# Kernel tuning notes

Hardware: AMD Instinct MI355X
Metric: run time of the kernel (lower is better)

Reference implementation:

```python
import jax, jax.numpy as jnp
import numpy as np

B, P, N, D = 32, 100, 1000, 128
SQRT_D = 11.313708498984761
CLIP = 10.0


def setup_inputs() -> dict:
    key = jax.random.key(0)
    ks = jax.random.split(key, 8)
    s = 1.0 / np.sqrt(D)  # keep k ~ N(0,1) so exp(k) is stable
    return {
        "encoded_nodes": jax.random.normal(ks[0], (B, N, D), jnp.float32),
        "encoded_q1": jax.random.normal(ks[1], (B, P, D), jnp.float32),
        "encoded_last_node": jax.random.normal(ks[2], (B, P, D), jnp.float32),
        "cur_dist": jax.random.uniform(ks[3], (B, P, N), jnp.float32),
        "ninf_mask": jnp.zeros((B, P, N), jnp.float32),
        "log_scale": jnp.ones((1,), jnp.float32),
        "Wq_first": jax.random.normal(ks[4], (D, D), jnp.float32) * s,
        "Wq_last": jax.random.normal(ks[5], (D, D), jnp.float32) * s,
        "Wk": jax.random.normal(ks[6], (D, D), jnp.float32) * s,
        "Wv": jax.random.normal(ks[7], (D, D), jnp.float32) * s,
        "dist_alpha_1": jnp.ones((1,), jnp.float32),
        "AFT_dist_alpha_1": jnp.ones((1,), jnp.float32),
    }


def reference(encoded_nodes, encoded_q1, encoded_last_node, cur_dist, ninf_mask,
              log_scale, Wq_first, Wq_last, Wk, Wv, dist_alpha_1, AFT_dist_alpha_1):
    # set_kv / set_q1 (torch Linear: x @ W.T)
    k = jnp.einsum('bnd,ed->bne', encoded_nodes, Wk)          # [B,N,D]
    v = jnp.einsum('bnd,ed->bne', encoded_nodes, Wv)          # [B,N,D]
    q_first = jnp.einsum('bpd,ed->bpe', encoded_q1, Wq_first) # [B,P,D]
    q_last = jnp.einsum('bpd,ed->bpe', encoded_last_node, Wq_last)
    q = q_first + q_last

    cur_dist_out = -cur_dist                                   # [B,P,N]
    bias_scale = log_scale * AFT_dist_alpha_1 * cur_dist_out + ninf_mask
    ebias = jnp.exp(bias_scale)                                # [B,P,N]
    ek = jnp.exp(k)                                            # [B,N,D]
    num = jnp.einsum('bpn,bnd->bpd', ebias, ek * v)
    den = jnp.einsum('bpn,bnd->bpd', ebias, ek)
    aft_out = jax.nn.sigmoid(q) * (num / den)                  # [B,P,D]

    score = jnp.einsum('bpd,bnd->bpn', aft_out, encoded_nodes) / SQRT_D
    score = score + log_scale * dist_alpha_1 * cur_dist_out
    score = CLIP * jnp.tanh(score) + ninf_mask
    return jax.nn.softmax(score, axis=2)
```

## Files before the change

kernel.cpp:

```cpp
#include <hip/hip_runtime.h>
#include <hip/hip_bf16.h>
#include <math.h>

#define B 32
#define P 100
#define N 1000
#define D 128

constexpr float SQRT_D_INV = 1.0f / 11.313708498984761f;
constexpr float CLIPV = 10.0f;

__device__ __forceinline__ void fma4(float4& a, float s, const float4& b) {
    a.x = fmaf(s, b.x, a.x);
    a.y = fmaf(s, b.y, a.y);
    a.z = fmaf(s, b.z, a.z);
    a.w = fmaf(s, b.w, a.w);
}

#define TT 64
__global__ __launch_bounds__(256) void prep_kernel(
        const float* __restrict__ nodes,
        const float* __restrict__ Wk,  const float* __restrict__ Wv,
        const float* __restrict__ Wqf, const float* __restrict__ Wql,
        float* __restrict__ wkT,  float* __restrict__ wvT,
        float* __restrict__ wqfT, float* __restrict__ wqlT,
        float* __restrict__ nodesT) {
    const int t = threadIdx.x;
    if (blockIdx.x < D) {
        const int e = blockIdx.x;
        const int d = t & 127;
        if ((t >> 7) == 0) {
            wkT[e * D + d] = Wk[d * D + e];
            wvT[e * D + d] = Wv[d * D + e];
        } else {
            wqfT[e * D + d] = Wqf[d * D + e];
            wqlT[e * D + d] = Wql[d * D + e];
        }
        return;
    }
    __shared__ float sh[TT][D + 1];
    const int blk = blockIdx.x - D;
    const int ntiles = (N + TT - 1) / TT;
    const int b  = blk / ntiles;
    const int n0 = (blk % ntiles) * TT;
    const int rows = min(TT, N - n0);

    const float4* src = (const float4*)(nodes + ((long)b * N + n0) * D);
    for (int i = t; i < rows * (D / 4); i += 256) {
        int r = i >> 5, c = i & 31;
        float4 v = src[(long)r * (D / 4) + c];
        sh[r][c * 4 + 0] = v.x; sh[r][c * 4 + 1] = v.y;
        sh[r][c * 4 + 2] = v.z; sh[r][c * 4 + 3] = v.w;
    }
    __syncthreads();

    const int nl = t & 63;
    const int eg = t >> 6;
    if (nl < rows) {
        #pragma unroll
        for (int k = 0; k < 32; ++k) {
            int e = eg * 32 + k;
            nodesT[((long)b * D + e) * N + n0 + nl] = sh[nl][e];
        }
    }
}

#define R1 32
__global__ __launch_bounds__(256) void kv_kernel(
        const float* __restrict__ nodes,
        const float* __restrict__ wkT,
        const float* __restrict__ wvT,
        float* __restrict__ ek,
        float* __restrict__ ekv) {
    __shared__ float sh[R1][D];
    const int t = threadIdx.x;
    const int dq = t & 31;
    const int rl = t >> 5;
    const long row0 = (long)blockIdx.x * R1;

    const float4* src = (const float4*)(nodes + row0 * D);
    float4* dst = (float4*)(&sh[0][0]);
    #pragma unroll
    for (int i = 0; i < (R1 * D / 4) / 256; ++i)
        dst[t + i * 256] = src[t + i * 256];
    __syncthreads();

    float4 ka[4], va[4];
    #pragma unroll
    for (int rr = 0; rr < 4; ++rr) {
        ka[rr] = make_float4(0.f, 0.f, 0.f, 0.f);
        va[rr] = make_float4(0.f, 0.f, 0.f, 0.f);
    }

    const float* wkp = wkT + dq * 4;
    const float* wvp = wvT + dq * 4;

    float4 cwk[4], cwv[4];
    #pragma unroll
    for (int ee = 0; ee < 4; ++ee) {
        cwk[ee] = *(const float4*)(wkp + ee * D);
        cwv[ee] = *(const float4*)(wvp + ee * D);
    }

    for (int e0 = 0; e0 < D; e0 += 4) {
        float4 nwk[4], nwv[4];
        if (e0 + 4 < D) {
            #pragma unroll
            for (int ee = 0; ee < 4; ++ee) {
                nwk[ee] = *(const float4*)(wkp + (e0 + 4 + ee) * D);
                nwv[ee] = *(const float4*)(wvp + (e0 + 4 + ee) * D);
            }
        }
        #pragma unroll
        for (int rr = 0; rr < 4; ++rr) {
            float4 s4 = *(const float4*)(&sh[rl * 4 + rr][e0]);
            fma4(ka[rr], s4.x, cwk[0]); fma4(ka[rr], s4.y, cwk[1]);
            fma4(ka[rr], s4.z, cwk[2]); fma4(ka[rr], s4.w, cwk[3]);
            fma4(va[rr], s4.x, cwv[0]); fma4(va[rr], s4.y, cwv[1]);
            fma4(va[rr], s4.z, cwv[2]); fma4(va[rr], s4.w, cwv[3]);
        }
        #pragma unroll
        for (int ee = 0; ee < 4; ++ee) { cwk[ee] = nwk[ee]; cwv[ee] = nwv[ee]; }
    }

    #pragma unroll
    for (int rr = 0; rr < 4; ++rr) {
        long row = row0 + rl * 4 + rr;
        float4 e4;
        e4.x = __expf(ka[rr].x); e4.y = __expf(ka[rr].y);
        e4.z = __expf(ka[rr].z); e4.w = __expf(ka[rr].w);
        float4 ev;
        ev.x = e4.x * va[rr].x; ev.y = e4.y * va[rr].y;
        ev.z = e4.z * va[rr].z; ev.w = e4.w * va[rr].w;
        *(float4*)(ek + row * D + dq * 4) = e4;
        *(float4*)(ekv + row * D + dq * 4) = ev;
    }
}

#define R2 16
__global__ __launch_bounds__(256) void q_kernel(
        const float* __restrict__ q1,
        const float* __restrict__ qlast,
        const float* __restrict__ wqfT,
        const float* __restrict__ wqlT,
        float* __restrict__ qsig) {
    __shared__ float sh1[R2][D];
    __shared__ float sh2[R2][D];
    const int t = threadIdx.x;
    const int dq = t & 31;
    const int rl = t >> 5;
    const long row0 = (long)blockIdx.x * R2;

    const float4* s1 = (const float4*)(q1 + row0 * D);
    const float4* s2 = (const float4*)(qlast + row0 * D);
    float4* d1 = (float4*)(&sh1[0][0]);
    float4* d2 = (float4*)(&sh2[0][0]);
    #pragma unroll
    for (int i = 0; i < (R2 * D / 4) / 256; ++i) {
        d1[t + i * 256] = s1[t + i * 256];
        d2[t + i * 256] = s2[t + i * 256];
    }
    __syncthreads();

    float4 acc[2];
    acc[0] = make_float4(0.f, 0.f, 0.f, 0.f);
    acc[1] = make_float4(0.f, 0.f, 0.f, 0.f);

    const float* wfp = wqfT + dq * 4;
    const float* wlp = wqlT + dq * 4;

    float4 cwf[4], cwl[4];
    #pragma unroll
    for (int ee = 0; ee < 4; ++ee) {
        cwf[ee] = *(const float4*)(wfp + ee * D);
        cwl[ee] = *(const float4*)(wlp + ee * D);
    }

    for (int e0 = 0; e0 < D; e0 += 4) {
        float4 nwf[4], nwl[4];
        if (e0 + 4 < D) {
            #pragma unroll
            for (int ee = 0; ee < 4; ++ee) {
                nwf[ee] = *(const float4*)(wfp + (e0 + 4 + ee) * D);
                nwl[ee] = *(const float4*)(wlp + (e0 + 4 + ee) * D);
            }
        }
        #pragma unroll
        for (int rr = 0; rr < 2; ++rr) {
            float4 a4 = *(const float4*)(&sh1[rl * 2 + rr][e0]);
            float4 b4 = *(const float4*)(&sh2[rl * 2 + rr][e0]);
            fma4(acc[rr], a4.x, cwf[0]); fma4(acc[rr], a4.y, cwf[1]);
            fma4(acc[rr], a4.z, cwf[2]); fma4(acc[rr], a4.w, cwf[3]);
            fma4(acc[rr], b4.x, cwl[0]); fma4(acc[rr], b4.y, cwl[1]);
            fma4(acc[rr], b4.z, cwl[2]); fma4(acc[rr], b4.w, cwl[3]);
        }
        #pragma unroll
        for (int ee = 0; ee < 4; ++ee) { cwf[ee] = nwf[ee]; cwl[ee] = nwl[ee]; }
    }

    #pragma unroll
    for (int rr = 0; rr < 2; ++rr) {
        long row = row0 + rl * 2 + rr;
        float4 s;
        s.x = 1.0f / (1.0f + __expf(-acc[rr].x));
        s.y = 1.0f / (1.0f + __expf(-acc[rr].y));
        s.z = 1.0f / (1.0f + __expf(-acc[rr].z));
        s.w = 1.0f / (1.0f + __expf(-acc[rr].w));
        *(float4*)(qsig + row * D + dq * 4) = s;
    }
}

#define PT 20
#define TS3 16

#define GLDS(gsrc, ldst) __builtin_amdgcn_global_load_lds( \
    (const __attribute__((address_space(1))) void*)(gsrc), \
    (__attribute__((address_space(3))) void*)(ldst), 16, 0, 0)

__global__ __launch_bounds__(128) void aft_part_kernel(
        const float* __restrict__ cur_dist,
        const float* __restrict__ ninf,
        const float* __restrict__ ek,
        const float* __restrict__ ekv,
        const float* __restrict__ log_scale,
        const float* __restrict__ aft_alpha,
        float* __restrict__ pnum,
        float* __restrict__ pden,
        int NC, int L) {
    __shared__ __align__(16) float ekL[2][TS3 * D];
    __shared__ __align__(16) float evL[2][TS3 * D];
    __shared__ __align__(16) float eb[2][TS3][33];
    const int t = threadIdx.x;
    const int lane = t & 63;
    const int wid = t >> 6;
    const int dq4 = (t & 31) * 4;
    const int pl = t >> 5;
    const int pl5 = pl * 5;
    const int b    = blockIdx.x % B;
    const int rest = blockIdx.x / B;
    const int c    = rest % NC;
    const int pt   = rest / NC;
    const int p0 = pt * PT;
    const int n_begin = c * L;
    const int n_end = min(N, n_begin + L);
    const float lsA = log_scale[0] * aft_alpha[0];

    float4 num[5], den[5];
    #pragma unroll
    for (int i = 0; i < 5; ++i) {
        num[i] = make_float4(0.f, 0.f, 0.f, 0.f);
        den[i] = make_float4(0.f, 0.f, 0.f, 0.f);
    }

    const float* ekc = ek  + (long)b * N * D;
    const float* evc = ekv + (long)b * N * D;

    int n0 = n_begin;
    int ts = min(TS3, n_end - n0);

    {
        const float* gk = ekc + (long)n0 * D;
        const float* gv = evc + (long)n0 * D;
        for (int i = wid; i < ts / 2; i += 2) {
            GLDS(gk + i * 256 + lane * 4, &ekL[0][i * 256]);
            GLDS(gv + i * 256 + lane * 4, &evL[0][i * 256]);
        }
    }
    float rv[3];
    #pragma unroll
    for (int k = 0; k < 3; ++k) {
        int s = t + k * 128;
        int pp = s >> 4, nl = s & 15;
        rv[k] = 0.f;
        if (s < PT * TS3 && nl < ts) {
            long idx = ((long)b * P + p0 + pp) * N + (n0 + nl);
            rv[k] = fmaf(-lsA, cur_dist[idx], ninf[idx]);
        }
    }

    int cur = 0;
    while (n0 < n_end) {
        #pragma unroll
        for (int k = 0; k < 3; ++k) {
            int s = t + k * 128;
            int pp = s >> 4, nl = s & 15;
            if (s < PT * TS3 && nl < ts) eb[cur][nl][pp] = __expf(rv[k]);
        }
        __syncthreads();

        const int n0n = n0 + ts;
        const int tsn = min(TS3, n_end - n0n);
        if (n0n < n_end) {
            const float* gk = ekc + (long)n0n * D;
            const float* gv = evc + (long)n0n * D;
            for (int i = wid; i < tsn / 2; i += 2) {
                GLDS(gk + i * 256 + lane * 4, &ekL[cur ^ 1][i * 256]);
                GLDS(gv + i * 256 + lane * 4, &evL[cur ^ 1][i * 256]);
            }
            #pragma unroll
            for (int k = 0; k < 3; ++k) {
                int s = t + k * 128;
                int pp = s >> 4, nl = s & 15;
                rv[k] = 0.f;
                if (s < PT * TS3 && nl < tsn) {
                    long idx = ((long)b * P + p0 + pp) * N + (n0n + nl);
                    rv[k] = fmaf(-lsA, cur_dist[idx], ninf[idx]);
                }
            }
        }

        const float* ekp = &ekL[cur][dq4];
        const float* evp = &evL[cur][dq4];
        #pragma unroll 4
        for (int j = 0; j < ts; ++j) {
            float4 ekq = *(const float4*)(ekp + j * D);
            float4 evq = *(const float4*)(evp + j * D);
            float e0 = eb[cur][j][pl5 + 0];
            float e1 = eb[cur][j][pl5 + 1];
            float e2 = eb[cur][j][pl5 + 2];
            float e3 = eb[cur][j][pl5 + 3];
            float e4 = eb[cur][j][pl5 + 4];
            fma4(num[0], e0, evq); fma4(den[0], e0, ekq);
            fma4(num[1], e1, evq); fma4(den[1], e1, ekq);
            fma4(num[2], e2, evq); fma4(den[2], e2, ekq);
            fma4(num[3], e3, evq); fma4(den[3], e3, ekq);
            fma4(num[4], e4, evq); fma4(den[4], e4, ekq);
        }
        cur ^= 1;
        n0 = n0n;
        ts = tsn;
    }

    #pragma unroll
    for (int r = 0; r < 5; ++r) {
        int p = p0 + pl5 + r;
        long o = (((long)c * B + b) * P + p) * D + dq4;
        *(float4*)(pnum + o) = num[r];
        *(float4*)(pden + o) = den[r];
    }
}

__global__ __launch_bounds__(256) void aft_reduce_kernel(
        const float* __restrict__ pnum,
        const float* __restrict__ pden,
        const float* __restrict__ qsig,
        float* __restrict__ aft,
        int NC) {
    const long i = ((long)blockIdx.x * 256 + threadIdx.x) * 4;
    const long BPD = (long)B * P * D;
    float4 n = make_float4(0.f, 0.f, 0.f, 0.f);
    float4 d = make_float4(0.f, 0.f, 0.f, 0.f);
    int c = 0;
    for (; c + 2 <= NC; c += 2) {
        float4 a0 = *(const float4*)(pnum + (long)c * BPD + i);
        float4 a1 = *(const float4*)(pnum + (long)(c + 1) * BPD + i);
        float4 b0 = *(const float4*)(pden + (long)c * BPD + i);
        float4 b1 = *(const float4*)(pden + (long)(c + 1) * BPD + i);
        n.x += a0.x + a1.x; n.y += a0.y + a1.y;
        n.z += a0.z + a1.z; n.w += a0.w + a1.w;
        d.x += b0.x + b1.x; d.y += b0.y + b1.y;
        d.z += b0.z + b1.z; d.w += b0.w + b1.w;
    }
    if (c < NC) {
        float4 a0 = *(const float4*)(pnum + (long)c * BPD + i);
        float4 b0 = *(const float4*)(pden + (long)c * BPD + i);
        n.x += a0.x; n.y += a0.y; n.z += a0.z; n.w += a0.w;
        d.x += b0.x; d.y += b0.y; d.z += b0.z; d.w += b0.w;
    }
    float4 q = *(const float4*)(qsig + i);
    float4 o;
    o.x = q.x * n.x / d.x;
    o.y = q.y * n.y / d.y;
    o.z = q.z * n.z / d.z;
    o.w = q.w * n.w / d.w;
    *(float4*)(aft + i) = o;
}

#define PT2 10
#define SC 4
__global__ __launch_bounds__(128) void score_part_kernel(
        const float* __restrict__ aft,
        const float* __restrict__ nodesT,
        const float* __restrict__ cur_dist,
        const float* __restrict__ ninf,
        const float* __restrict__ log_scale,
        const float* __restrict__ dist_alpha,
        float* __restrict__ out,
        float* __restrict__ sums) {
    __shared__ float sa[PT2][D];
    __shared__ float red[2][PT2];
    const int t = threadIdx.x;
    const int wid = t >> 6;
    const int b    = blockIdx.x % B;
    const int rest = blockIdx.x / B;
    const int c    = rest % SC;
    const int pt   = rest / SC;
    const int p0 = pt * PT2;
    const float lsA = log_scale[0] * dist_alpha[0];

    for (int i = t; i < PT2 * D; i += 128) {
        sa[i >> 7][i & 127] = aft[((long)b * P + p0) * D + i];
    }
    __syncthreads();

    const int n0 = c * 256 + t * 2;
    const bool act = (n0 < N);
    const int ncl = act ? n0 : 0;
    const float* ntb = nodesT + (long)b * D * N;

    float2 acc[PT2];
    #pragma unroll
    for (int i = 0; i < PT2; ++i) acc[i] = make_float2(0.f, 0.f);

    float2 cx[4];
    #pragma unroll
    for (int ee = 0; ee < 4; ++ee)
        cx[ee] = *(const float2*)(ntb + (long)ee * N + ncl);

    for (int e0 = 0; e0 < D; e0 += 4) {
        float2 nx[4];
        if (e0 + 4 < D) {
            #pragma unroll
            for (int ee = 0; ee < 4; ++ee)
                nx[ee] = *(const float2*)(ntb + (long)(e0 + 4 + ee) * N + ncl);
        }
        #pragma unroll
        for (int i = 0; i < PT2; ++i) {
            float4 a4 = *(const float4*)(&sa[i][e0]);
            acc[i].x = fmaf(cx[0].x, a4.x, acc[i].x);
            acc[i].x = fmaf(cx[1].x, a4.y, acc[i].x);
            acc[i].x = fmaf(cx[2].x, a4.z, acc[i].x);
            acc[i].x = fmaf(cx[3].x, a4.w, acc[i].x);
            acc[i].y = fmaf(cx[0].y, a4.x, acc[i].y);
            acc[i].y = fmaf(cx[1].y, a4.y, acc[i].y);
            acc[i].y = fmaf(cx[2].y, a4.z, acc[i].y);
            acc[i].y = fmaf(cx[3].y, a4.w, acc[i].y);
        }
        #pragma unroll
        for (int ee = 0; ee < 4; ++ee) cx[ee] = nx[ee];
    }

    #pragma unroll
    for (int i = 0; i < PT2; ++i) {
        float2 ev = make_float2(0.f, 0.f);
        if (act) {
            long idx = ((long)b * P + p0 + i) * N + n0;
            float2 cd = *(const float2*)(cur_dist + idx);
            float2 nf = *(const float2*)(ninf + idx);
            float sx = fmaf(acc[i].x, SQRT_D_INV, -lsA * cd.x);
            float sy = fmaf(acc[i].y, SQRT_D_INV, -lsA * cd.y);
            float ax = fabsf(sx), ay = fabsf(sy);
            float rx = 1.f - 2.f / (__expf(2.f * ax) + 1.f);
            float ry = 1.f - 2.f / (__expf(2.f * ay) + 1.f);
            float scx = CLIPV * copysignf(rx, sx) + nf.x;
            float scy = CLIPV * copysignf(ry, sy) + nf.y;
            ev.x = __expf(scx);
            ev.y = __expf(scy);
            *(float2*)(out + idx) = ev;
        }
        float s = ev.x + ev.y;
        #pragma unroll
        for (int o = 1; o < 64; o <<= 1) s += __shfl_xor(s, o, 64);
        if ((t & 63) == 0) red[wid][i] = s;
    }
    __syncthreads();
    if (t < PT2) {
        atomicAdd(&sums[b * P + p0 + t], red[0][t] + red[1][t]);
    }
}

__global__ __launch_bounds__(256) void normalize_kernel(
        float* __restrict__ out, const float* __restrict__ sums) {
    const int row = blockIdx.x;
    const int t = threadIdx.x;
    const float inv = 1.0f / sums[row];
    float4* r = (float4*)(out + (long)row * N);
    if (t < N / 4) {
        float4 v = r[t];
        v.x *= inv; v.y *= inv; v.z *= inv; v.w *= inv;
        r[t] = v;
    }
}

extern "C" void kernel_launch(void* const* d_in, const int* in_sizes, int n_in,
                              void* d_out, int out_size, void* d_ws, size_t ws_size,
                              hipStream_t stream) {
    const float* nodes      = (const float*)d_in[0];
    const float* q1         = (const float*)d_in[1];
    const float* qlast      = (const float*)d_in[2];
    const float* cur_dist   = (const float*)d_in[3];
    const float* ninf       = (const float*)d_in[4];
    const float* log_scale  = (const float*)d_in[5];
    const float* Wqf        = (const float*)d_in[6];
    const float* Wql        = (const float*)d_in[7];
    const float* Wk         = (const float*)d_in[8];
    const float* Wv         = (const float*)d_in[9];
    const float* dist_alpha = (const float*)d_in[10];
    const float* aft_alpha  = (const float*)d_in[11];
    float* out = (float*)d_out;

    const long BND = (long)B * N * D;
    const long BPD = (long)B * P * D;
    const long W2  = (long)D * D;

    float* ws     = (float*)d_ws;
    float* ek     = ws;
    float* ekv    = ek + BND;
    float* qsig   = ekv + BND;
    float* aft    = qsig + BPD;
    float* wkT    = aft + BPD;
    float* wvT    = wkT + W2;
    float* wqfT   = wvT + W2;
    float* wqlT   = wqfT + W2;
    float* nodesT = wqlT + W2;
    float* sums   = nodesT + BND;
    float* pnum   = sums + (long)B * P;

    long avail = (long)(ws_size / 4) - (3 * BND + 2 * BPD + 4 * W2 + (long)B * P);
    int NC = (int)(avail / (2 * BPD));
    if (NC < 1) NC = 1;
    if (NC > 12) NC = 12;
    int L = (((N + NC - 1) / NC) + 3) & ~3;
    NC = (N + L - 1) / L;
    float* pden = pnum + (long)NC * BPD;

    hipMemsetAsync(sums, 0, (size_t)B * P * sizeof(float), stream);
    prep_kernel<<<D + B * ((N + TT - 1) / TT), 256, 0, stream>>>(
        nodes, Wk, Wv, Wqf, Wql, wkT, wvT, wqfT, wqlT, nodesT);
    kv_kernel<<<(B * N) / R1, 256, 0, stream>>>(nodes, wkT, wvT, ek, ekv);
    q_kernel<<<(B * P) / R2, 256, 0, stream>>>(q1, qlast, wqfT, wqlT, qsig);
    aft_part_kernel<<<B * (P / PT) * NC, 128, 0, stream>>>(
        cur_dist, ninf, ek, ekv, log_scale, aft_alpha, pnum, pden, NC, L);
    aft_reduce_kernel<<<(int)(BPD / 1024), 256, 0, stream>>>(pnum, pden, qsig, aft, NC);
    score_part_kernel<<<B * SC * (P / PT2), 128, 0, stream>>>(
        aft, nodesT, cur_dist, ninf, log_scale, dist_alpha, out, sums);
    normalize_kernel<<<B * P, 256, 0, stream>>>(out, sums);
}
```

Measured before the change: 249.4 us.

## Split AFT node tiles across two thread halves, read ek/ekv directly from global

The AFT partial kernel now uses 256 threads, with each half handling 16 of a 32-node tile. ek and ekv are read directly from global memory (served by cache) instead of being staged into LDS with global_load_lds, so only the exp-bias tile stays in shared memory. The two halves' num/den partials are then reduced through shared memory before being written out. The score kernel's per-block P tile is also halved to launch more blocks. This trades LDS traffic and occupancy limits for more global/L2 load pressure and extra reduction syncs.

```diff
diff --git a/kernel.cpp b/kernel.cpp
--- a/kernel.cpp
+++ b/kernel.cpp
@@ -211,13 +211,10 @@
 }
 
 #define PT 20
-#define TS3 16
-
-#define GLDS(gsrc, ldst) __builtin_amdgcn_global_load_lds( \
-    (const __attribute__((address_space(1))) void*)(gsrc), \
-    (__attribute__((address_space(3))) void*)(ldst), 16, 0, 0)
-
-__global__ __launch_bounds__(128) void aft_part_kernel(
+#define TS 32
+#define EBS 672
+
+__global__ __launch_bounds__(256, 8) void aft_part_kernel(
         const float* __restrict__ cur_dist,
         const float* __restrict__ ninf,
         const float* __restrict__ ek,
@@ -227,14 +224,11 @@
         float* __restrict__ pnum,
         float* __restrict__ pden,
         int NC, int L) {
-    __shared__ __align__(16) float ekL[2][TS3 * D];
-    __shared__ __align__(16) float evL[2][TS3 * D];
-    __shared__ __align__(16) float eb[2][TS3][33];
+    __shared__ __align__(16) float smem[2560];
     const int t = threadIdx.x;
-    const int lane = t & 63;
-    const int wid = t >> 6;
-    const int dq4 = (t & 31) * 4;
-    const int pl = t >> 5;
+    const int dq = t & 31;
+    const int pl = (t >> 5) & 3;
+    const int h  = t >> 7;
     const int pl5 = pl * 5;
     const int b    = blockIdx.x % B;
     const int rest = blockIdx.x / B;
@@ -252,91 +246,106 @@
         den[i] = make_float4(0.f, 0.f, 0.f, 0.f);
     }
 
-    const float* ekc = ek  + (long)b * N * D;
-    const float* evc = ekv + (long)b * N * D;
-
+    const float* ekb = ek  + (long)b * N * D + dq * 4;
+    const float* evb = ekv + (long)b * N * D + dq * 4;
+
+    float rv[3];
     int n0 = n_begin;
-    int ts = min(TS3, n_end - n0);
-
-    {
-        const float* gk = ekc + (long)n0 * D;
-        const float* gv = evc + (long)n0 * D;
-        for (int i = wid; i < ts / 2; i += 2) {
-            GLDS(gk + i * 256 + lane * 4, &ekL[0][i * 256]);
-            GLDS(gv + i * 256 + lane * 4, &evL[0][i * 256]);
-        }
-    }
-    float rv[3];
+    int ts = min(TS, n_end - n0);
+
     #pragma unroll
     for (int k = 0; k < 3; ++k) {
-        int s = t + k * 128;
-        int pp = s >> 4, nl = s & 15;
+        int s = t + k * 256;
+        int pp = s >> 5, nl = s & 31;
         rv[k] = 0.f;
-        if (s < PT * TS3 && nl < ts) {
+        if (s < PT * TS && nl < ts) {
             long idx = ((long)b * P + p0 + pp) * N + (n0 + nl);
             rv[k] = fmaf(-lsA, cur_dist[idx], ninf[idx]);
         }
     }
 
-    int cur = 0;
+    int buf = 0;
     while (n0 < n_end) {
         #pragma unroll
         for (int k = 0; k < 3; ++k) {
-            int s = t + k * 128;
-            int pp = s >> 4, nl = s & 15;
-            if (s < PT * TS3 && nl < ts) eb[cur][nl][pp] = __expf(rv[k]);
+            int s = t + k * 256;
+            int pp = s >> 5, nl = s & 31;
+            if (s < PT * TS && nl < ts) smem[buf * EBS + nl * 21 + pp] = __expf(rv[k]);
         }
         __syncthreads();
 
         const int n0n = n0 + ts;
-        const int tsn = min(TS3, n_end - n0n);
+        const int tsn = min(TS, n_end - n0n);
         if (n0n < n_end) {
-            const float* gk = ekc + (long)n0n * D;
-            const float* gv = evc + (long)n0n * D;
-            for (int i = wid; i < tsn / 2; i += 2) {
-                GLDS(gk + i * 256 + lane * 4, &ekL[cur ^ 1][i * 256]);
-                GLDS(gv + i * 256 + lane * 4, &evL[cur ^ 1][i * 256]);
-            }
             #pragma unroll
             for (int k = 0; k < 3; ++k) {
-                int s = t + k * 128;
-                int pp = s >> 4, nl = s & 15;
+                int s = t + k * 256;
+                int pp = s >> 5, nl = s & 31;
                 rv[k] = 0.f;
-                if (s < PT * TS3 && nl < tsn) {
+                if (s < PT * TS && nl < tsn) {
                     long idx = ((long)b * P + p0 + pp) * N + (n0n + nl);
                     rv[k] = fmaf(-lsA, cur_dist[idx], ninf[idx]);
                 }
             }
         }
 
-        const float* ekp = &ekL[cur][dq4];
-        const float* evp = &evL[cur][dq4];
+        const int jmax = min(16, ts - h * 16);
+        const float* ekp = ekb + (long)(n0 + h * 16) * D;
+        const float* evp = evb + (long)(n0 + h * 16) * D;
+        const float* ebt = smem + buf * EBS + (h * 16) * 21 + pl5;
         #pragma unroll 4
-        for (int j = 0; j < ts; ++j) {
-            float4 ekq = *(const float4*)(ekp + j * D);
-            float4 evq = *(const float4*)(evp + j * D);
-            float e0 = eb[cur][j][pl5 + 0];
-            float e1 = eb[cur][j][pl5 + 1];
-            float e2 = eb[cur][j][pl5 + 2];
-            float e3 = eb[cur][j][pl5 + 3];
-            float e4 = eb[cur][j][pl5 + 4];
+        for (int j = 0; j < jmax; ++j) {
+            float4 ekq = *(const float4*)(ekp + (long)j * D);
+            float4 evq = *(const float4*)(evp + (long)j * D);
+            float e0 = ebt[j * 21 + 0];
+            float e1 = ebt[j * 21 + 1];
+            float e2 = ebt[j * 21 + 2];
+            float e3 = ebt[j * 21 + 3];
+            float e4 = ebt[j * 21 + 4];
             fma4(num[0], e0, evq); fma4(den[0], e0, ekq);
             fma4(num[1], e1, evq); fma4(den[1], e1, ekq);
             fma4(num[2], e2, evq); fma4(den[2], e2, ekq);
             fma4(num[3], e3, evq); fma4(den[3], e3, ekq);
             fma4(num[4], e4, evq); fma4(den[4], e4, ekq);
         }
-        cur ^= 1;
+        buf ^= 1;
         n0 = n0n;
         ts = tsn;
     }
 
-    #pragma unroll
-    for (int r = 0; r < 5; ++r) {
-        int p = p0 + pl5 + r;
-        long o = (((long)c * B + b) * P + p) * D + dq4;
-        *(float4*)(pnum + o) = num[r];
-        *(float4*)(pden + o) = den[r];
+    __syncthreads();
+    if (h == 1) {
+        const int i = t - 128;
+        #pragma unroll
+        for (int r = 0; r < 5; ++r)
+            *(float4*)&smem[i * 20 + r * 4] = num[r];
+    }
+    __syncthreads();
+    if (h == 0) {
+        #pragma unroll
+        for (int r = 0; r < 5; ++r) {
+            float4 o = *(const float4*)&smem[t * 20 + r * 4];
+            num[r].x += o.x; num[r].y += o.y; num[r].z += o.z; num[r].w += o.w;
+            long oidx = (((long)c * B + b) * P + (p0 + pl5 + r)) * D + dq * 4;
+            *(float4*)(pnum + oidx) = num[r];
+        }
+    }
+    __syncthreads();
+    if (h == 1) {
+        const int i = t - 128;
+        #pragma unroll
+        for (int r = 0; r < 5; ++r)
+            *(float4*)&smem[i * 20 + r * 4] = den[r];
+    }
+    __syncthreads();
+    if (h == 0) {
+        #pragma unroll
+        for (int r = 0; r < 5; ++r) {
+            float4 o = *(const float4*)&smem[t * 20 + r * 4];
+            den[r].x += o.x; den[r].y += o.y; den[r].z += o.z; den[r].w += o.w;
+            long oidx = (((long)c * B + b) * P + (p0 + pl5 + r)) * D + dq * 4;
+            *(float4*)(pden + oidx) = den[r];
+        }
     }
 }
 
@@ -376,7 +385,7 @@
     *(float4*)(aft + i) = o;
 }
 
-#define PT2 10
+#define PT2 5
 #define SC 4
 __global__ __launch_bounds__(128) void score_part_kernel(
         const float* __restrict__ aft,
@@ -529,7 +538,7 @@
         nodes, Wk, Wv, Wqf, Wql, wkT, wvT, wqfT, wqlT, nodesT);
     kv_kernel<<<(B * N) / R1, 256, 0, stream>>>(nodes, wkT, wvT, ek, ekv);
     q_kernel<<<(B * P) / R2, 256, 0, stream>>>(q1, qlast, wqfT, wqlT, qsig);
-    aft_part_kernel<<<B * (P / PT) * NC, 128, 0, stream>>>(
+    aft_part_kernel<<<B * (P / PT) * NC, 256, 0, stream>>>(
         cur_dist, ninf, ek, ekv, log_scale, aft_alpha, pnum, pden, NC, L);
     aft_reduce_kernel<<<(int)(BPD / 1024), 256, 0, stream>>>(pnum, pden, qsig, aft, NC);
     score_part_kernel<<<B * SC * (P / PT2), 128, 0, stream>>>(
```

New measurement: 653.3 us. +161.9%, slower.
